# Performance work log

Hardware: AMD Instinct MI355X
Metric: run time of the kernel (lower is better)

Reference implementation:

```python
import jax, jax.numpy as jnp
import numpy as np

D_MODEL = 1024
NUM_HEADS = 16
HEAD_DIM = D_MODEL // NUM_HEADS


def setup_inputs() -> dict:
    key = jax.random.key(0)
    ks = jax.random.split(key, 9)
    B, S = 4, 2048
    s = 1.0 / np.sqrt(D_MODEL)
    return {
        "x": jax.random.normal(ks[0], (B, S, D_MODEL), dtype=jnp.float32),
        "Wq": jax.random.normal(ks[1], (D_MODEL, D_MODEL), dtype=jnp.float32) * s,
        "bq": jnp.zeros((D_MODEL,), dtype=jnp.float32),
        "Wk": jax.random.normal(ks[2], (D_MODEL, D_MODEL), dtype=jnp.float32) * s,
        "bk": jnp.zeros((D_MODEL,), dtype=jnp.float32),
        "Wv": jax.random.normal(ks[3], (D_MODEL, D_MODEL), dtype=jnp.float32) * s,
        "bv": jnp.zeros((D_MODEL,), dtype=jnp.float32),
        "Wo": jax.random.normal(ks[4], (D_MODEL, D_MODEL), dtype=jnp.float32) * s,
        "bo": jnp.zeros((D_MODEL,), dtype=jnp.float32),
    }


def reference(x, Wq, bq, Wk, bk, Wv, bv, Wo, bo):
    B, S, D = x.shape
    H, Hd = NUM_HEADS, HEAD_DIM
    # projections: [B,S,D] -> [B,H,S,Hd]
    def split_heads(t):
        return t.reshape(B, S, H, Hd).transpose(0, 2, 1, 3)
    q = split_heads(x @ Wq + bq)
    k = split_heads(x @ Wk + bk)
    v = split_heads(x @ Wv + bv)
    scale = 1.0 / jnp.sqrt(jnp.asarray(Hd, dtype=x.dtype))
    scores = jnp.einsum("bhsd,bhtd->bhst", q, k) * scale  # [B,H,S,S]
    attn = jax.nn.softmax(scores, axis=-1)
    ctx = jnp.einsum("bhst,bhtd->bhsd", attn, v)  # [B,H,S,Hd]
    ctx = ctx.transpose(0, 2, 1, 3).reshape(B, S, D)
    return ctx @ Wo + bo
```

## Files before the change

### kernel.cpp

```cpp
#include <hip/hip_runtime.h>
#include <hip/hip_bf16.h>
#include <stdint.h>


typedef __bf16 bf16;
typedef __bf16 bf16x8 __attribute__((ext_vector_type(8)));
typedef float  f32x4  __attribute__((ext_vector_type(4)));
typedef float  f32x16 __attribute__((ext_vector_type(16)));

#define XB_OFF   (0ull)
#define WT_OFF   (16ull << 20)
#define Q_OFF    (24ull << 20)
#define K_OFF    (40ull << 20)
#define V_OFF    (56ull << 20)
#define CTX_OFF  (72ull << 20)

#define QSCALE 0.18033688011112042591f

__device__ __forceinline__ void gload_lds16(const void* g, void* l) {
  __builtin_amdgcn_global_load_lds(
      (const __attribute__((address_space(1))) void*)g,
      (__attribute__((address_space(3))) void*)l, 16, 0, 0);
}

__global__ __launch_bounds__(256) void cvt_x(const float* __restrict__ x,
                                             bf16* __restrict__ xb) {
  int i = blockIdx.x * 256 + threadIdx.x;
  const float4* p = (const float4*)x;
  float4 a = p[(size_t)i * 2];
  float4 b = p[(size_t)i * 2 + 1];
  bf16x8 o;
  o[0] = (bf16)a.x; o[1] = (bf16)a.y; o[2] = (bf16)a.z; o[3] = (bf16)a.w;
  o[4] = (bf16)b.x; o[5] = (bf16)b.y; o[6] = (bf16)b.z; o[7] = (bf16)b.w;
  *((bf16x8*)xb + i) = o;
}

__global__ __launch_bounds__(256) void cvt_w(const float* __restrict__ w0,
                                             const float* __restrict__ w1,
                                             const float* __restrict__ w2,
                                             const float* __restrict__ w3,
                                             bf16* __restrict__ wt) {
  int z = blockIdx.z;
  const float* W = (z == 0) ? w0 : (z == 1) ? w1 : (z == 2) ? w2 : w3;
  bf16* Wt = wt + (size_t)z * 1024 * 1024;
  __shared__ float tile[64][65];
  int i0 = blockIdx.y * 64, o0 = blockIdx.x * 64;
  int tid = threadIdx.x;
#pragma unroll
  for (int rep = 0; rep < 16; rep++) {
    int idx = rep * 256 + tid;
    int r = idx >> 6, c = idx & 63;
    tile[r][c] = W[(size_t)(i0 + r) * 1024 + o0 + c];
  }
  __syncthreads();
#pragma unroll
  for (int rep = 0; rep < 16; rep++) {
    int idx = rep * 256 + tid;
    int r = idx >> 6, c = idx & 63;
    Wt[(size_t)(o0 + r) * 1024 + i0 + c] = (bf16)tile[c][r];
  }
}

template <int MODE>
__global__ __launch_bounds__(256, 2) void gemm_bt(
    const bf16* __restrict__ A, const bf16* __restrict__ Bt,
    const float* __restrict__ b0, const float* __restrict__ b1,
    const float* __restrict__ b2,
    bf16* __restrict__ Qo, bf16* __restrict__ Ko, bf16* __restrict__ Vo,
    float* __restrict__ out) {
  __shared__ __align__(16) bf16 a_lds[128 * 64];
  __shared__ __align__(16) bf16 b_lds[128 * 64];
  int tid = threadIdx.x;
  int lane = tid & 63, wid = tid >> 6;
  int wr = wid >> 1, wc = wid & 1;
  int g = lane >> 4, rlo = lane & 15;
  int m0 = blockIdx.x * 128, n0 = blockIdx.y * 128;

  f32x4 acc[4][4] = {};
  const char* Ab = (const char*)A;
  const char* Bb = (const char*)Bt;

  for (int k0 = 0; k0 < 1024; k0 += 64) {
#pragma unroll
    for (int rep = 0; rep < 4; rep++) {
      int idx = rep * 256 + tid;
      int row = idx >> 3;
      int sw = ((idx & 7) * 16) ^ ((row & 7) << 4);
      gload_lds16(Ab + ((size_t)(m0 + row) * 1024 + k0) * 2 + sw,
                  (char*)a_lds + (size_t)idx * 16);
    }
#pragma unroll
    for (int rep = 0; rep < 4; rep++) {
      int idx = rep * 256 + tid;
      int row = idx >> 3;
      int sw = ((idx & 7) * 16) ^ ((row & 7) << 4);
      gload_lds16(Bb + ((size_t)(n0 + row) * 1024 + k0) * 2 + sw,
                  (char*)b_lds + (size_t)idx * 16);
    }
    __syncthreads();
#pragma unroll
    for (int ks = 0; ks < 2; ks++) {
      bf16x8 af[4], bfr[4];
#pragma unroll
      for (int mt = 0; mt < 4; mt++) {
        int row = wr * 64 + mt * 16 + rlo;
        int koff = (ks * 32 + g * 8) ^ ((row & 7) << 3);
        af[mt] = *(const bf16x8*)&a_lds[row * 64 + koff];
      }
#pragma unroll
      for (int nt = 0; nt < 4; nt++) {
        int row = wc * 64 + nt * 16 + rlo;
        int koff = (ks * 32 + g * 8) ^ ((row & 7) << 3);
        bfr[nt] = *(const bf16x8*)&b_lds[row * 64 + koff];
      }
#pragma unroll
      for (int mt = 0; mt < 4; mt++)
#pragma unroll
        for (int nt = 0; nt < 4; nt++)
          acc[mt][nt] = __builtin_amdgcn_mfma_f32_16x16x32_bf16(
              af[mt], bfr[nt], acc[mt][nt], 0, 0, 0);
    }
    __syncthreads();
  }

#pragma unroll
  for (int nt = 0; nt < 4; nt++) {
    int n = n0 + wc * 64 + nt * 16 + rlo;
    if (MODE == 0) {
      int which = n >> 10, nn = n & 1023;
      const float* bp = (which == 0) ? b0 : (which == 1) ? b1 : b2;
      float bias = bp[nn];
      bf16* dst = (which == 0) ? Qo : (which == 1) ? Ko : Vo;
      float scale = (which == 0) ? QSCALE : 1.0f;
      int h = nn >> 6, hd = nn & 63;
#pragma unroll
      for (int mt = 0; mt < 4; mt++) {
#pragma unroll
        for (int r = 0; r < 4; r++) {
          int m = m0 + wr * 64 + mt * 16 + g * 4 + r;
          int bb = m >> 11, ss = m & 2047;
          float v = (acc[mt][nt][r] + bias) * scale;
          dst[(((size_t)(bb * 16 + h) * 2048 + ss) << 6) + hd] = (bf16)v;
        }
      }
    } else {
      float bias = b0[n];
#pragma unroll
      for (int mt = 0; mt < 4; mt++) {
#pragma unroll
        for (int r = 0; r < 4; r++) {
          int m = m0 + wr * 64 + mt * 16 + g * 4 + r;
          out[(size_t)m * 1024 + n] = acc[mt][nt][r] + bias;
        }
      }
    }
  }
}

__global__ __launch_bounds__(256) void vtr(const bf16* __restrict__ V,
                                           bf16* __restrict__ Vt) {
  __shared__ bf16 t[64][72];
  int bh = blockIdx.y, s0 = blockIdx.x * 64;
  int tid = threadIdx.x;
  const bf16* Vb = V + ((size_t)bh * 2048 + s0) * 64;
  bf16* Tb = Vt + (size_t)bh * 64 * 2048;
#pragma unroll
  for (int rep = 0; rep < 2; rep++) {
    int idx = rep * 256 + tid;
    int s = idx >> 3, dv = (idx & 7) * 8;
    bf16x8 v = *(const bf16x8*)&Vb[(size_t)s * 64 + dv];
#pragma unroll
    for (int j = 0; j < 8; j++) t[s][dv + j] = v[j];
  }
  __syncthreads();
#pragma unroll
  for (int rep = 0; rep < 2; rep++) {
    int idx = rep * 256 + tid;
    int d = idx >> 3, sc = (idx & 7) * 8;
    bf16x8 v;
#pragma unroll
    for (int j = 0; j < 8; j++) {
      int sl = sc + j;
      int sp = (sl & ~12) | ((sl & 4) << 1) | ((sl & 8) >> 1);
      v[j] = t[sp][d];
    }
    *(bf16x8*)&Tb[(size_t)d * 2048 + s0 + sc] = v;
  }
}

__global__ __launch_bounds__(256, 4) void attn(const bf16* __restrict__ Q,
                                               const bf16* __restrict__ K,
                                               const bf16* __restrict__ Vt,
                                               bf16* __restrict__ ctx) {
  __shared__ __align__(16) bf16 kbuf[3][32 * 64];
  __shared__ __align__(16) bf16 vbuf[3][64 * 32];
  int tid = threadIdx.x;
  int lane = tid & 63, wid = tid >> 6;
  int r31 = lane & 31, half = lane >> 5;
  int wg = blockIdx.x;
  int virt = (wg & 7) * 128 + (wg >> 3);
  int bh = virt >> 4, qt = virt & 15;
  int qbase = qt * 128 + wid * 32;

  const char* Kg = (const char*)(K + (size_t)bh * 2048 * 64);
  const char* Vg = (const char*)(Vt + (size_t)bh * 64 * 2048);

  int krow = tid >> 3;
  size_t kofs = (size_t)krow * 128 + (((tid & 7) ^ (krow & 7)) << 4);
  int vrow = tid >> 2;
  size_t vofs = (size_t)vrow * 4096 + (((tid & 3) ^ (vrow & 3)) << 4);

  int kread[4];
#pragma unroll
  for (int ks = 0; ks < 4; ks++)
    kread[ks] = r31 * 64 + (((2 * ks + half) ^ (r31 & 7)) << 3);
  int vread[2][2];
#pragma unroll
  for (int dh = 0; dh < 2; dh++)
#pragma unroll
    for (int ks = 0; ks < 2; ks++)
      vread[dh][ks] = (dh * 32 + r31) * 32 +
                      ((((2 * ks + half) & 3) ^ (r31 & 3)) << 3);

  const bf16* qrow = Q + ((size_t)bh * 2048 + qbase + r31) * 64 + half * 8;
  bf16x8 qa[4];
#pragma unroll
  for (int ks = 0; ks < 4; ks++) qa[ks] = *(const bf16x8*)&qrow[ks * 16];

  f32x16 o0 = {}, o1 = {};
  f32x4 lvec = {};

#define STAGE(BUF, T0)                                                        \
  do {                                                                        \
    gload_lds16(Kg + (size_t)(T0) * 128 + kofs, (char*)kbuf[BUF] + tid * 16); \
    gload_lds16(Vg + (size_t)(T0) * 2 + vofs, (char*)vbuf[BUF] + tid * 16);   \
  } while (0)

  STAGE(0, 0);
  STAGE(1, 32);
  asm volatile("s_waitcnt vmcnt(2)" ::: "memory");
  __builtin_amdgcn_s_barrier();

  int cs = 0;
  for (int it = 0; it < 64; ++it) {
    int sb = cs + 2 - ((cs >= 1) ? 3 : 0);
    STAGE(sb, ((it + 2) & 63) * 32);

    const bf16* kb = kbuf[cs];
    const bf16* vb = vbuf[cs];

    f32x16 s = {};
    __builtin_amdgcn_s_setprio(1);
#pragma unroll
    for (int ks = 0; ks < 4; ks++) {
      bf16x8 kf = *(const bf16x8*)&kb[kread[ks]];
      s = __builtin_amdgcn_mfma_f32_32x32x16_bf16(kf, qa[ks], s, 0, 0, 0);
    }
    __builtin_amdgcn_s_setprio(0);

    bf16x8 v00 = *(const bf16x8*)&vb[vread[0][0]];
    bf16x8 v01 = *(const bf16x8*)&vb[vread[0][1]];
    bf16x8 v10 = *(const bf16x8*)&vb[vread[1][0]];
    bf16x8 v11 = *(const bf16x8*)&vb[vread[1][1]];

#pragma unroll
    for (int i = 0; i < 16; i++) s[i] = __builtin_amdgcn_exp2f(s[i]);
#pragma unroll
    for (int i = 0; i < 4; i++)
      lvec[i] += (s[i] + s[i + 4]) + (s[i + 8] + s[i + 12]);

    bf16x8 pa0, pa1;
#pragma unroll
    for (int i = 0; i < 8; i++) {
      pa0[i] = (bf16)s[i];
      pa1[i] = (bf16)s[8 + i];
    }

    __builtin_amdgcn_s_setprio(1);
    o0 = __builtin_amdgcn_mfma_f32_32x32x16_bf16(pa0, v00, o0, 0, 0, 0);
    o0 = __builtin_amdgcn_mfma_f32_32x32x16_bf16(pa1, v01, o0, 0, 0, 0);
    o1 = __builtin_amdgcn_mfma_f32_32x32x16_bf16(pa0, v10, o1, 0, 0, 0);
    o1 = __builtin_amdgcn_mfma_f32_32x32x16_bf16(pa1, v11, o1, 0, 0, 0);
    __builtin_amdgcn_s_setprio(0);

    asm volatile("s_waitcnt vmcnt(2)" ::: "memory");
    __builtin_amdgcn_s_barrier();

    cs = (cs == 2) ? 0 : cs + 1;
  }
#undef STAGE

  float l = (lvec[0] + lvec[1]) + (lvec[2] + lvec[3]);
  l += __shfl_xor(l, 32);
  float inv = 1.0f / l;
  int b = bh >> 4, h = bh & 15;
#pragma unroll
  for (int r = 0; r < 16; r++) {
    int ql = (r & 3) + 8 * (r >> 2) + 4 * half;
    float iv = __shfl(inv, ql);
    size_t base = (((size_t)(b * 2048 + qbase + ql)) << 10) + h * 64 + r31;
    ctx[base] = (bf16)(o0[r] * iv);
    ctx[base + 32] = (bf16)(o1[r] * iv);
  }
}

extern "C" void kernel_launch(void* const* d_in, const int* in_sizes, int n_in,
                              void* d_out, int out_size, void* d_ws, size_t ws_size,
                              hipStream_t stream) {
  const float* x  = (const float*)d_in[0];
  const float* Wq = (const float*)d_in[1];
  const float* bq = (const float*)d_in[2];
  const float* Wk = (const float*)d_in[3];
  const float* bk = (const float*)d_in[4];
  const float* Wv = (const float*)d_in[5];
  const float* bv = (const float*)d_in[6];
  const float* Wo = (const float*)d_in[7];
  const float* bo = (const float*)d_in[8];
  float* out = (float*)d_out;
  char* ws = (char*)d_ws;

  bf16* xb  = (bf16*)(ws + XB_OFF);
  bf16* wt  = (bf16*)(ws + WT_OFF);
  bf16* Qb  = (bf16*)(ws + Q_OFF);
  bf16* Kb  = (bf16*)(ws + K_OFF);
  bf16* Vb  = (bf16*)(ws + V_OFF);
  bf16* cx  = (bf16*)(ws + CTX_OFF);
  bf16* Vtb = (bf16*)(ws + XB_OFF);

  cvt_x<<<4096, 256, 0, stream>>>(x, xb);
  cvt_w<<<dim3(16, 16, 4), 256, 0, stream>>>(Wq, Wk, Wv, Wo, wt);
  gemm_bt<0><<<dim3(64, 24), 256, 0, stream>>>(xb, wt, bq, bk, bv,
                                               Qb, Kb, Vb, nullptr);
  vtr<<<dim3(32, 64), 256, 0, stream>>>(Vb, Vtb);
  attn<<<1024, 256, 0, stream>>>(Qb, Kb, Vtb, cx);
  gemm_bt<1><<<dim3(64, 8), 256, 0, stream>>>(cx, wt + 3ull * 1024 * 1024, bo,
                                              nullptr, nullptr, nullptr,
                                              nullptr, nullptr, out);
}
```

Measured before the change: 180.2 us.

## Shrink attention blocks to two waves and use double-buffered K/V staging

The attention kernel now launches 2048 workgroups of 128 threads, each covering 64 query rows instead of 128, so each thread issues two async global-to-LDS loads per K and V tile. The triple-buffer ring with partial vmcnt waits is replaced by a simple double buffer synchronized with __syncthreads each iteration. The aim is more blocks per CU and better load balance with less LDS per block. In exchange, K/V traffic per query row doubles and the full barrier waits on all outstanding loads, which can expose memory latency.

```diff
diff --git a/kernel.cpp b/kernel.cpp
--- a/kernel.cpp
+++ b/kernel.cpp
@@ -188,27 +188,28 @@
   }
 }
 
-__global__ __launch_bounds__(256, 4) void attn(const bf16* __restrict__ Q,
+__global__ __launch_bounds__(128, 4) void attn(const bf16* __restrict__ Q,
                                                const bf16* __restrict__ K,
                                                const bf16* __restrict__ Vt,
                                                bf16* __restrict__ ctx) {
-  __shared__ __align__(16) bf16 kbuf[3][32 * 64];
-  __shared__ __align__(16) bf16 vbuf[3][64 * 32];
+  __shared__ __align__(16) bf16 kbuf[2][32 * 64];
+  __shared__ __align__(16) bf16 vbuf[2][64 * 32];
   int tid = threadIdx.x;
   int lane = tid & 63, wid = tid >> 6;
   int r31 = lane & 31, half = lane >> 5;
   int wg = blockIdx.x;
-  int virt = (wg & 7) * 128 + (wg >> 3);
-  int bh = virt >> 4, qt = virt & 15;
-  int qbase = qt * 128 + wid * 32;
+  int virt = (wg & 7) * 256 + (wg >> 3);
+  int bh = virt >> 5, qt = virt & 31;
+  int qbase = qt * 64 + wid * 32;
 
   const char* Kg = (const char*)(K + (size_t)bh * 2048 * 64);
   const char* Vg = (const char*)(Vt + (size_t)bh * 64 * 2048);
 
-  int krow = tid >> 3;
-  size_t kofs = (size_t)krow * 128 + (((tid & 7) ^ (krow & 7)) << 4);
-  int vrow = tid >> 2;
-  size_t vofs = (size_t)vrow * 4096 + (((tid & 3) ^ (vrow & 3)) << 4);
+  int i0 = tid, i1 = tid + 128;
+  size_t kofs0 = (size_t)(i0 >> 3) * 128 + (((i0 & 7) ^ ((i0 >> 3) & 7)) << 4);
+  size_t kofs1 = (size_t)(i1 >> 3) * 128 + (((i1 & 7) ^ ((i1 >> 3) & 7)) << 4);
+  size_t vofs0 = (size_t)(i0 >> 2) * 4096 + (((i0 & 3) ^ ((i0 >> 2) & 3)) << 4);
+  size_t vofs1 = (size_t)(i1 >> 2) * 4096 + (((i1 & 3) ^ ((i1 >> 2) & 3)) << 4);
 
   int kread[4];
 #pragma unroll
@@ -232,22 +233,25 @@
 
 #define STAGE(BUF, T0)                                                        \
   do {                                                                        \
-    gload_lds16(Kg + (size_t)(T0) * 128 + kofs, (char*)kbuf[BUF] + tid * 16); \
-    gload_lds16(Vg + (size_t)(T0) * 2 + vofs, (char*)vbuf[BUF] + tid * 16);   \
+    gload_lds16(Kg + (size_t)(T0) * 128 + kofs0,                              \
+                (char*)kbuf[BUF] + tid * 16);                                 \
+    gload_lds16(Kg + (size_t)(T0) * 128 + kofs1,                              \
+                (char*)kbuf[BUF] + 2048 + tid * 16);                          \
+    gload_lds16(Vg + (size_t)(T0) * 2 + vofs0,                                \
+                (char*)vbuf[BUF] + tid * 16);                                 \
+    gload_lds16(Vg + (size_t)(T0) * 2 + vofs1,                                \
+                (char*)vbuf[BUF] + 2048 + tid * 16);                          \
   } while (0)
 
   STAGE(0, 0);
-  STAGE(1, 32);
-  asm volatile("s_waitcnt vmcnt(2)" ::: "memory");
-  __builtin_amdgcn_s_barrier();
-
-  int cs = 0;
+  __syncthreads();
+
+  int cur = 0;
   for (int it = 0; it < 64; ++it) {
-    int sb = cs + 2 - ((cs >= 1) ? 3 : 0);
-    STAGE(sb, ((it + 2) & 63) * 32);
-
-    const bf16* kb = kbuf[cs];
-    const bf16* vb = vbuf[cs];
+    STAGE(cur ^ 1, ((it + 1) & 63) * 32);
+
+    const bf16* kb = kbuf[cur];
+    const bf16* vb = vbuf[cur];
 
     f32x16 s = {};
     __builtin_amdgcn_s_setprio(1);
@@ -283,10 +287,8 @@
     o1 = __builtin_amdgcn_mfma_f32_32x32x16_bf16(pa1, v11, o1, 0, 0, 0);
     __builtin_amdgcn_s_setprio(0);
 
-    asm volatile("s_waitcnt vmcnt(2)" ::: "memory");
-    __builtin_amdgcn_s_barrier();
-
-    cs = (cs == 2) ? 0 : cs + 1;
+    __syncthreads();
+    cur ^= 1;
   }
 #undef STAGE
 
@@ -332,7 +334,7 @@
   gemm_bt<0><<<dim3(64, 24), 256, 0, stream>>>(xb, wt, bq, bk, bv,
                                                Qb, Kb, Vb, nullptr);
   vtr<<<dim3(32, 64), 256, 0, stream>>>(Vb, Vtb);
-  attn<<<1024, 256, 0, stream>>>(Qb, Kb, Vtb, cx);
+  attn<<<2048, 128, 0, stream>>>(Qb, Kb, Vtb, cx);
   gemm_bt<1><<<dim3(64, 8), 256, 0, stream>>>(cx, wt + 3ull * 1024 * 1024, bo,
                                               nullptr, nullptr, nullptr,
                                               nullptr, nullptr, out);
```

New measurement: 190.7 us. +5.8%, slower.
